# Kernel optimization log

Measured on AMD Instinct MI355X. Metric: run time of the kernel, lower is better.

The kernel has to match this reference:

```python
import jax, jax.numpy as jnp
import numpy as np
import math

B, N, H, D = 2, 2048, 16, 64

def setup_inputs() -> dict:
    key = jax.random.key(0)
    kq, kk, kv = jax.random.split(key, 3)
    q = jax.random.normal(kq, (B, N, H, D), dtype=jnp.float32)
    k = jax.random.normal(kk, (B, N, H, D), dtype=jnp.float32)
    v = jax.random.normal(kv, (B, N, H, D), dtype=jnp.float32)
    return {"q": q, "k": k, "v": v}

def reference(q, k, v):
    # world_size == 1 path: standard full attention.
    d = q.shape[-1]
    scale = 1.0 / math.sqrt(d)
    # [b, h, nq, nk]
    scores = jnp.einsum("bqhd,bkhd->bhqk", q, k) * scale
    attn = jax.nn.softmax(scores, axis=-1)
    out = jnp.einsum("bhqk,bkhd->bqhd", attn, v)
    return out
```

## Files before the change

kernel.cpp:

```cpp
#include <hip/hip_runtime.h>
#include <hip/hip_bf16.h>
#include <math.h>

typedef __bf16 bf16x8 __attribute__((ext_vector_type(8)));
typedef float  f32x4  __attribute__((ext_vector_type(4)));

#define B_    2
#define N_    2048
#define H_    16
#define D_    64
#define HD    (H_ * D_)
#define QSCALE (0.125f * 1.44269504089f)
#define THR   8.0f
#define NT    32
#define TILE_BYTES 16384
#define BH_BYTES ((size_t)NT * TILE_BYTES)
#define WS_NEED ((size_t)B_ * H_ * BH_BYTES)

#if __has_builtin(__builtin_amdgcn_exp2f)
#define EXP2F(x) __builtin_amdgcn_exp2f(x)
#else
#define EXP2F(x) __expf(0.69314718056f * (x))
#endif

__global__ __launch_bounds__(256) void prep_kv(
    const float* __restrict__ k, const float* __restrict__ v,
    char* __restrict__ ws)
{
    __shared__ float tile[64][68];
    const int tid = threadIdx.x;
    const int bid = blockIdx.x;

    if (bid < 1024) {
        int bh = bid >> 5, t = bid & 31;
        int b = bh >> 4, h = bh & 15;
        char* dst = ws + (size_t)bh * BH_BYTES + (size_t)t * TILE_BYTES;
        #pragma unroll
        for (int p = 0; p < 2; ++p) {
            int d16 = (tid & 3) + p * 4;
            int n   = tid >> 2;
            const float* s = k + ((size_t)(b * N_ + t * 64 + n) * H_ + h) * D_ + d16 * 8;
            f32x4 a0 = *(const f32x4*)s;
            f32x4 a1 = *(const f32x4*)(s + 4);
            bf16x8 o;
            #pragma unroll
            for (int j = 0; j < 4; ++j) { o[j] = (__bf16)a0[j]; o[4 + j] = (__bf16)a1[j]; }
            int chunk = n * 8 + (d16 ^ (n & 7));
            *(bf16x8*)(dst + chunk * 16) = o;
        }
    } else {
        int vb = bid - 1024;
        int bh = vb >> 5, t = vb & 31;
        int b = bh >> 4, h = bh & 15;
        #pragma unroll
        for (int rep = 0; rep < 4; ++rep) {
            int idx = rep * 256 + tid;
            int i = idx >> 4, c4 = (idx & 15) * 4;
            *(f32x4*)&tile[i][c4] =
                *(const f32x4*)(v + ((size_t)(b * N_ + t * 64 + i) * H_ + h) * D_ + c4);
        }
        __syncthreads();
        char* dst = ws + (size_t)bh * BH_BYTES + (size_t)t * TILE_BYTES + 8192;
        #pragma unroll
        for (int rep = 0; rep < 2; ++rep) {
            int idx = rep * 256 + tid;
            int d = idx >> 3, n16 = idx & 7;
            bf16x8 o;
            #pragma unroll
            for (int j = 0; j < 8; ++j) o[j] = (__bf16)tile[n16 * 8 + j][d];
            int chunk = d * 8 + (n16 ^ (d & 7));
            *(bf16x8*)(dst + chunk * 16) = o;
        }
    }
}

__global__ __launch_bounds__(512, 4) void attn_fwd_v4(
    const float* __restrict__ q,
    const char* __restrict__ ws,
    float* __restrict__ out)
{
    const int tid  = threadIdx.x;
    const int lane = tid & 63;
    const int w    = tid >> 6;
    const int lo   = lane & 15;
    const int hi   = lane >> 4;

    int bid = blockIdx.x;
    int wg  = (bid & 7) * 64 + (bid >> 3);
    int qt  = wg & 15;
    int bh  = wg >> 4;
    int h   = bh & 15;
    int b   = bh >> 4;

    __shared__ __align__(16) char kv_lds[2][TILE_BYTES];
    __shared__ __align__(16) __bf16 p_lds[8][16][72];

    const char* wsrc = ws + (size_t)bh * BH_BYTES;
    const int q0 = qt * 128 + w * 16;

    bf16x8 qa[2];
    #pragma unroll
    for (int kk = 0; kk < 2; ++kk) {
        const float* qs = q + ((size_t)(b * N_ + q0 + lo) * H_ + h) * D_ + kk * 32 + hi * 8;
        f32x4 a0 = *(const f32x4*)qs;
        f32x4 a1 = *(const f32x4*)(qs + 4);
        #pragma unroll
        for (int j = 0; j < 4; ++j) {
            qa[kk][j]     = (__bf16)(a0[j] * QSCALE);
            qa[kk][4 + j] = (__bf16)(a1[j] * QSCALE);
        }
    }

    float m[4], l[4];
    f32x4 o[4];
    #pragma unroll
    for (int r = 0; r < 4; ++r) { m[r] = -INFINITY; l[r] = 0.f; }
    #pragma unroll
    for (int f = 0; f < 4; ++f) o[f] = (f32x4)0.f;

    const int soff = w * 2048 + lane * 16;

    {
        bf16x8 s0 = *(const bf16x8*)(wsrc + soff);
        bf16x8 s1 = *(const bf16x8*)(wsrc + soff + 1024);
        *(bf16x8*)(kv_lds[0] + soff) = s0;
        *(bf16x8*)(kv_lds[0] + soff + 1024) = s1;
    }
    __syncthreads();

    for (int t = 0; t < NT; ++t) {
        const char* kbuf = kv_lds[t & 1];
        const char* vbuf = kbuf + 8192;

        int tn = (t + 1) & (NT - 1);
        bf16x8 s0 = *(const bf16x8*)(wsrc + (size_t)tn * TILE_BYTES + soff);
        bf16x8 s1 = *(const bf16x8*)(wsrc + (size_t)tn * TILE_BYTES + soff + 1024);

        f32x4 sc[4];
        #pragma unroll
        for (int c = 0; c < 4; ++c) {
            sc[c] = (f32x4)0.f;
            #pragma unroll
            for (int kk = 0; kk < 2; ++kk) {
                int row = c * 16 + lo;
                int d16 = kk * 4 + hi;
                bf16x8 kf = *(const bf16x8*)(kbuf + row * 128 + ((d16 ^ (row & 7)) << 4));
                sc[c] = __builtin_amdgcn_mfma_f32_16x16x32_bf16(qa[kk], kf, sc[c], 0, 0, 0);
            }
        }
        bf16x8 vf[4][2];
        #pragma unroll
        for (int f = 0; f < 4; ++f)
            #pragma unroll
            for (int s2 = 0; s2 < 2; ++s2) {
                int row = f * 16 + lo;
                int n16 = s2 * 4 + hi;
                vf[f][s2] = *(const bf16x8*)(vbuf + row * 128 + ((n16 ^ (row & 7)) << 4));
            }

        float pm[4];
        #pragma unroll
        for (int r = 0; r < 4; ++r)
            pm[r] = fmaxf(fmaxf(sc[0][r], sc[1][r]), fmaxf(sc[2][r], sc[3][r]));
        int ok = (pm[0] <= m[0] + THR) & (pm[1] <= m[1] + THR)
               & (pm[2] <= m[2] + THR) & (pm[3] <= m[3] + THR);
        if (!__all(ok)) {
            #pragma unroll
            for (int r = 0; r < 4; ++r) {
                float tmax = pm[r];
                #pragma unroll
                for (int msk = 1; msk <= 8; msk <<= 1)
                    tmax = fmaxf(tmax, __shfl_xor(tmax, msk, 64));
                float mn = fmaxf(m[r], tmax);
                float a  = EXP2F(m[r] - mn);
                m[r] = mn;
                l[r] *= a;
                #pragma unroll
                for (int f = 0; f < 4; ++f) o[f][r] *= a;
            }
        }
        #pragma unroll
        for (int r = 0; r < 4; ++r) {
            float p0 = EXP2F(sc[0][r] - m[r]);
            float p1 = EXP2F(sc[1][r] - m[r]);
            float p2 = EXP2F(sc[2][r] - m[r]);
            float p3 = EXP2F(sc[3][r] - m[r]);
            l[r] += (p0 + p1) + (p2 + p3);
            p_lds[w][hi * 4 + r][lo]      = (__bf16)p0;
            p_lds[w][hi * 4 + r][16 + lo] = (__bf16)p1;
            p_lds[w][hi * 4 + r][32 + lo] = (__bf16)p2;
            p_lds[w][hi * 4 + r][48 + lo] = (__bf16)p3;
        }
        __asm__ volatile("" ::: "memory");
        bf16x8 pa0 = *(const bf16x8*)&p_lds[w][lo][hi * 8];
        bf16x8 pa1 = *(const bf16x8*)&p_lds[w][lo][32 + hi * 8];
        __asm__ volatile("" ::: "memory");

        #pragma unroll
        for (int f = 0; f < 4; ++f) {
            o[f] = __builtin_amdgcn_mfma_f32_16x16x32_bf16(pa0, vf[f][0], o[f], 0, 0, 0);
            o[f] = __builtin_amdgcn_mfma_f32_16x16x32_bf16(pa1, vf[f][1], o[f], 0, 0, 0);
        }

        *(bf16x8*)(kv_lds[(t + 1) & 1] + soff) = s0;
        *(bf16x8*)(kv_lds[(t + 1) & 1] + soff + 1024) = s1;
        __syncthreads();
    }

    float* op = out + (size_t)b * N_ * HD + (size_t)h * D_;
    #pragma unroll
    for (int r = 0; r < 4; ++r) {
        float rs = l[r];
        #pragma unroll
        for (int msk = 1; msk <= 8; msk <<= 1)
            rs += __shfl_xor(rs, msk, 64);
        float rinv = 1.f / rs;
        float* orow = op + (size_t)(q0 + hi * 4 + r) * HD;
        #pragma unroll
        for (int f = 0; f < 4; ++f)
            orow[f * 16 + lo] = o[f][r] * rinv;
    }
}

__global__ __launch_bounds__(256) void attn_fwd_v1(
    const float* __restrict__ q, const float* __restrict__ k,
    const float* __restrict__ v, float* __restrict__ out)
{
    const int tid  = threadIdx.x;
    const int lane = tid & 63;
    const int w    = tid >> 6;
    const int lo   = lane & 15;
    const int hi   = lane >> 4;
    const int qt   = blockIdx.x;
    const int h    = blockIdx.y;
    const int b    = blockIdx.z;

    __shared__ __align__(16) __bf16 p_lds[4][16][40];

    const size_t bh_off = (size_t)b * N_ * HD + (size_t)h * D_;
    const float* qp = q + bh_off;
    const float* kp = k + bh_off;
    const float* vp = v + bh_off;
    float*       op = out + bh_off;

    const int q0 = qt * 64 + w * 16;

    bf16x8 qa[2];
    {
        const float* qrow = qp + (size_t)(q0 + lo) * HD + hi * 8;
        #pragma unroll
        for (int kk = 0; kk < 2; ++kk)
            #pragma unroll
            for (int j = 0; j < 8; ++j)
                qa[kk][j] = (__bf16)(qrow[kk * 32 + j] * 0.125f);
    }

    float m[4], l[4];
    f32x4 o[4];
    #pragma unroll
    for (int r = 0; r < 4; ++r) { m[r] = -INFINITY; l[r] = 0.f; }
    #pragma unroll
    for (int f = 0; f < 4; ++f) o[f] = (f32x4)0.f;

    for (int kv0 = 0; kv0 < N_; kv0 += 32) {
        f32x4 s[2];
        #pragma unroll
        for (int c = 0; c < 2; ++c) {
            s[c] = (f32x4)0.f;
            const float* krow = kp + (size_t)(kv0 + c * 16 + lo) * HD + hi * 8;
            #pragma unroll
            for (int kk = 0; kk < 2; ++kk) {
                bf16x8 kbv;
                #pragma unroll
                for (int j = 0; j < 8; ++j) kbv[j] = (__bf16)krow[kk * 32 + j];
                s[c] = __builtin_amdgcn_mfma_f32_16x16x32_bf16(qa[kk], kbv, s[c], 0, 0, 0);
            }
        }
        float alpha[4], p0[4], p1[4];
        #pragma unroll
        for (int r = 0; r < 4; ++r) {
            float t = fmaxf(s[0][r], s[1][r]);
            #pragma unroll
            for (int msk = 1; msk <= 8; msk <<= 1) t = fmaxf(t, __shfl_xor(t, msk, 64));
            float mn = fmaxf(m[r], t);
            alpha[r] = __expf(m[r] - mn);
            p0[r] = __expf(s[0][r] - mn);
            p1[r] = __expf(s[1][r] - mn);
            float rs = p0[r] + p1[r];
            #pragma unroll
            for (int msk = 1; msk <= 8; msk <<= 1) rs += __shfl_xor(rs, msk, 64);
            l[r] = l[r] * alpha[r] + rs;
            m[r] = mn;
        }
        #pragma unroll
        for (int f = 0; f < 4; ++f)
            #pragma unroll
            for (int r = 0; r < 4; ++r) o[f][r] *= alpha[r];
        #pragma unroll
        for (int r = 0; r < 4; ++r) {
            p_lds[w][hi * 4 + r][lo]      = (__bf16)p0[r];
            p_lds[w][hi * 4 + r][16 + lo] = (__bf16)p1[r];
        }
        __syncthreads();
        bf16x8 pa = *(const bf16x8*)&p_lds[w][lo][hi * 8];
        #pragma unroll
        for (int f = 0; f < 4; ++f) {
            const float* vrow = vp + (size_t)(kv0 + hi * 8) * HD + f * 16 + lo;
            bf16x8 vb;
            #pragma unroll
            for (int j = 0; j < 8; ++j) vb[j] = (__bf16)vrow[(size_t)j * HD];
            o[f] = __builtin_amdgcn_mfma_f32_16x16x32_bf16(pa, vb, o[f], 0, 0, 0);
        }
        __syncthreads();
    }
    #pragma unroll
    for (int r = 0; r < 4; ++r) {
        float rinv = 1.f / l[r];
        float* orow = op + (size_t)(q0 + hi * 4 + r) * HD;
        #pragma unroll
        for (int f = 0; f < 4; ++f) orow[f * 16 + lo] = o[f][r] * rinv;
    }
}

extern "C" void kernel_launch(void* const* d_in, const int* in_sizes, int n_in,
                              void* d_out, int out_size, void* d_ws, size_t ws_size,
                              hipStream_t stream)
{
    const float* q = (const float*)d_in[0];
    const float* k = (const float*)d_in[1];
    const float* v = (const float*)d_in[2];
    float* out = (float*)d_out;

    if (ws_size >= WS_NEED) {
        char* ws = (char*)d_ws;
        prep_kv<<<dim3(2048), 256, 0, stream>>>(k, v, ws);
        attn_fwd_v4<<<dim3(512), 512, 0, stream>>>(q, ws, out);
    } else {
        attn_fwd_v1<<<dim3(N_ / 64, H_, B_), 256, 0, stream>>>(q, k, v, out);
    }
}
```

Baseline: 148.0 us.

## Process two 16-row query blocks per wave to reuse K/V fragments

Each wave now handles 32 query rows (two 16-row blocks), so every K and V fragment read from LDS feeds twice as many MFMAs. The workgroup covers 256 queries, which halves the grid to 256 blocks and the per-block K/V staging traffic. The prep kernel now writes K/V without the swizzle, and the swizzle moves to the global-to-LDS copy in the attention kernel. The cost is roughly double the accumulator and score registers per wave (occupancy hint lowered from 4 to 2), and with only 256 blocks the GPU may be underfilled.

```diff
diff --git a/kernel.cpp b/kernel.cpp
--- a/kernel.cpp
+++ b/kernel.cpp
@@ -27,29 +27,27 @@
     const float* __restrict__ k, const float* __restrict__ v,
     char* __restrict__ ws)
 {
-    __shared__ float tile[64][68];
+    __shared__ float tile[64][69];
     const int tid = threadIdx.x;
     const int bid = blockIdx.x;
 
-    if (bid < 1024) {
-        int bh = bid >> 5, t = bid & 31;
+    if (bid < 2048) {
+        int g   = bid * 256 + tid;
+        int bh  = g >> 14;
+        int rem = g & 16383;
+        int t   = rem >> 9;
+        int c   = rem & 511;
+        int n   = c >> 3, d16 = c & 7;
         int b = bh >> 4, h = bh & 15;
-        char* dst = ws + (size_t)bh * BH_BYTES + (size_t)t * TILE_BYTES;
-        #pragma unroll
-        for (int p = 0; p < 2; ++p) {
-            int d16 = (tid & 3) + p * 4;
-            int n   = tid >> 2;
-            const float* s = k + ((size_t)(b * N_ + t * 64 + n) * H_ + h) * D_ + d16 * 8;
-            f32x4 a0 = *(const f32x4*)s;
-            f32x4 a1 = *(const f32x4*)(s + 4);
-            bf16x8 o;
-            #pragma unroll
-            for (int j = 0; j < 4; ++j) { o[j] = (__bf16)a0[j]; o[4 + j] = (__bf16)a1[j]; }
-            int chunk = n * 8 + (d16 ^ (n & 7));
-            *(bf16x8*)(dst + chunk * 16) = o;
-        }
+        const float* s = k + ((size_t)(b * N_ + t * 64 + n) * H_ + h) * D_ + d16 * 8;
+        f32x4 a0 = *(const f32x4*)s;
+        f32x4 a1 = *(const f32x4*)(s + 4);
+        bf16x8 o;
+        #pragma unroll
+        for (int j = 0; j < 4; ++j) { o[j] = (__bf16)a0[j]; o[4 + j] = (__bf16)a1[j]; }
+        *(bf16x8*)(ws + (size_t)bh * BH_BYTES + (size_t)t * TILE_BYTES + c * 16) = o;
     } else {
-        int vb = bid - 1024;
+        int vb = bid - 2048;
         int bh = vb >> 5, t = vb & 31;
         int b = bh >> 4, h = bh & 15;
         #pragma unroll
@@ -63,18 +61,17 @@
         char* dst = ws + (size_t)bh * BH_BYTES + (size_t)t * TILE_BYTES + 8192;
         #pragma unroll
         for (int rep = 0; rep < 2; ++rep) {
-            int idx = rep * 256 + tid;
-            int d = idx >> 3, n16 = idx & 7;
+            int c = rep * 256 + tid;
+            int d = c >> 3, n16 = c & 7;
             bf16x8 o;
             #pragma unroll
             for (int j = 0; j < 8; ++j) o[j] = (__bf16)tile[n16 * 8 + j][d];
-            int chunk = d * 8 + (n16 ^ (d & 7));
-            *(bf16x8*)(dst + chunk * 16) = o;
+            *(bf16x8*)(dst + c * 16) = o;
         }
     }
 }
 
-__global__ __launch_bounds__(512, 4) void attn_fwd_v4(
+__global__ __launch_bounds__(512, 2) void attn_fwd_v5(
     const float* __restrict__ q,
     const char* __restrict__ ws,
     float* __restrict__ out)
@@ -86,9 +83,9 @@
     const int hi   = lane >> 4;
 
     int bid = blockIdx.x;
-    int wg  = (bid & 7) * 64 + (bid >> 3);
-    int qt  = wg & 15;
-    int bh  = wg >> 4;
+    int wg  = (bid & 7) * 32 + (bid >> 3);
+    int qt  = wg & 7;
+    int bh  = wg >> 3;
     int h   = bh & 15;
     int b   = bh >> 4;
 
@@ -96,35 +93,44 @@
     __shared__ __align__(16) __bf16 p_lds[8][16][72];
 
     const char* wsrc = ws + (size_t)bh * BH_BYTES;
-    const int q0 = qt * 128 + w * 16;
-
-    bf16x8 qa[2];
-    #pragma unroll
-    for (int kk = 0; kk < 2; ++kk) {
-        const float* qs = q + ((size_t)(b * N_ + q0 + lo) * H_ + h) * D_ + kk * 32 + hi * 8;
-        f32x4 a0 = *(const f32x4*)qs;
-        f32x4 a1 = *(const f32x4*)(qs + 4);
-        #pragma unroll
-        for (int j = 0; j < 4; ++j) {
-            qa[kk][j]     = (__bf16)(a0[j] * QSCALE);
-            qa[kk][4 + j] = (__bf16)(a1[j] * QSCALE);
-        }
-    }
-
-    float m[4], l[4];
-    f32x4 o[4];
-    #pragma unroll
-    for (int r = 0; r < 4; ++r) { m[r] = -INFINITY; l[r] = 0.f; }
-    #pragma unroll
-    for (int f = 0; f < 4; ++f) o[f] = (f32x4)0.f;
-
-    const int soff = w * 2048 + lane * 16;
+    const int q0 = qt * 256 + w * 32;
+
+    const int srow = tid >> 3, scol = tid & 7;
+    const int src0 = (srow * 8 + (scol ^ (srow & 7))) * 16;
+    const int src1 = src0 + 8192;
+    const int ldso0 = tid * 16, ldso1 = tid * 16 + 8192;
+
+    bf16x8 qa[2][2];
+    #pragma unroll
+    for (int rb = 0; rb < 2; ++rb)
+        #pragma unroll
+        for (int kk = 0; kk < 2; ++kk) {
+            const float* qs = q + ((size_t)(b * N_ + q0 + rb * 16 + lo) * H_ + h) * D_ + kk * 32 + hi * 8;
+            f32x4 a0 = *(const f32x4*)qs;
+            f32x4 a1 = *(const f32x4*)(qs + 4);
+            #pragma unroll
+            for (int j = 0; j < 4; ++j) {
+                qa[rb][kk][j]     = (__bf16)(a0[j] * QSCALE);
+                qa[rb][kk][4 + j] = (__bf16)(a1[j] * QSCALE);
+            }
+        }
+
+    float m[2][4], l[2][4];
+    f32x4 o[2][4];
+    #pragma unroll
+    for (int rb = 0; rb < 2; ++rb)
+        #pragma unroll
+        for (int r = 0; r < 4; ++r) { m[rb][r] = -INFINITY; l[rb][r] = 0.f; }
+    #pragma unroll
+    for (int rb = 0; rb < 2; ++rb)
+        #pragma unroll
+        for (int f = 0; f < 4; ++f) o[rb][f] = (f32x4)0.f;
 
     {
-        bf16x8 s0 = *(const bf16x8*)(wsrc + soff);
-        bf16x8 s1 = *(const bf16x8*)(wsrc + soff + 1024);
-        *(bf16x8*)(kv_lds[0] + soff) = s0;
-        *(bf16x8*)(kv_lds[0] + soff + 1024) = s1;
+        bf16x8 s0 = *(const bf16x8*)(wsrc + src0);
+        bf16x8 s1 = *(const bf16x8*)(wsrc + src1);
+        *(bf16x8*)(kv_lds[0] + ldso0) = s0;
+        *(bf16x8*)(kv_lds[0] + ldso1) = s1;
     }
     __syncthreads();
 
@@ -132,22 +138,25 @@
         const char* kbuf = kv_lds[t & 1];
         const char* vbuf = kbuf + 8192;
 
-        int tn = (t + 1) & (NT - 1);
-        bf16x8 s0 = *(const bf16x8*)(wsrc + (size_t)tn * TILE_BYTES + soff);
-        bf16x8 s1 = *(const bf16x8*)(wsrc + (size_t)tn * TILE_BYTES + soff + 1024);
-
-        f32x4 sc[4];
-        #pragma unroll
-        for (int c = 0; c < 4; ++c) {
-            sc[c] = (f32x4)0.f;
+        const size_t tb = (size_t)((t + 1) & (NT - 1)) * TILE_BYTES;
+        bf16x8 s0 = *(const bf16x8*)(wsrc + tb + src0);
+        bf16x8 s1 = *(const bf16x8*)(wsrc + tb + src1);
+
+        f32x4 sc[2][4];
+        #pragma unroll
+        for (int rb = 0; rb < 2; ++rb)
+            #pragma unroll
+            for (int c = 0; c < 4; ++c) sc[rb][c] = (f32x4)0.f;
+        #pragma unroll
+        for (int c = 0; c < 4; ++c)
             #pragma unroll
             for (int kk = 0; kk < 2; ++kk) {
                 int row = c * 16 + lo;
                 int d16 = kk * 4 + hi;
                 bf16x8 kf = *(const bf16x8*)(kbuf + row * 128 + ((d16 ^ (row & 7)) << 4));
-                sc[c] = __builtin_amdgcn_mfma_f32_16x16x32_bf16(qa[kk], kf, sc[c], 0, 0, 0);
-            }
-        }
+                sc[0][c] = __builtin_amdgcn_mfma_f32_16x16x32_bf16(qa[0][kk], kf, sc[0][c], 0, 0, 0);
+                sc[1][c] = __builtin_amdgcn_mfma_f32_16x16x32_bf16(qa[1][kk], kf, sc[1][c], 0, 0, 0);
+            }
         bf16x8 vf[4][2];
         #pragma unroll
         for (int f = 0; f < 4; ++f)
@@ -158,68 +167,72 @@
                 vf[f][s2] = *(const bf16x8*)(vbuf + row * 128 + ((n16 ^ (row & 7)) << 4));
             }
 
-        float pm[4];
-        #pragma unroll
-        for (int r = 0; r < 4; ++r)
-            pm[r] = fmaxf(fmaxf(sc[0][r], sc[1][r]), fmaxf(sc[2][r], sc[3][r]));
-        int ok = (pm[0] <= m[0] + THR) & (pm[1] <= m[1] + THR)
-               & (pm[2] <= m[2] + THR) & (pm[3] <= m[3] + THR);
-        if (!__all(ok)) {
+        #pragma unroll
+        for (int rb = 0; rb < 2; ++rb) {
+            float pm[4];
+            #pragma unroll
+            for (int r = 0; r < 4; ++r)
+                pm[r] = fmaxf(fmaxf(sc[rb][0][r], sc[rb][1][r]), fmaxf(sc[rb][2][r], sc[rb][3][r]));
+            int ok = (pm[0] <= m[rb][0] + THR) & (pm[1] <= m[rb][1] + THR)
+                   & (pm[2] <= m[rb][2] + THR) & (pm[3] <= m[rb][3] + THR);
+            if (!__all(ok)) {
+                #pragma unroll
+                for (int r = 0; r < 4; ++r) {
+                    float tmax = pm[r];
+                    #pragma unroll
+                    for (int msk = 1; msk <= 8; msk <<= 1)
+                        tmax = fmaxf(tmax, __shfl_xor(tmax, msk, 64));
+                    float mn = fmaxf(m[rb][r], tmax);
+                    float a  = EXP2F(m[rb][r] - mn);
+                    m[rb][r] = mn;
+                    l[rb][r] *= a;
+                    #pragma unroll
+                    for (int f = 0; f < 4; ++f) o[rb][f][r] *= a;
+                }
+            }
             #pragma unroll
             for (int r = 0; r < 4; ++r) {
-                float tmax = pm[r];
-                #pragma unroll
-                for (int msk = 1; msk <= 8; msk <<= 1)
-                    tmax = fmaxf(tmax, __shfl_xor(tmax, msk, 64));
-                float mn = fmaxf(m[r], tmax);
-                float a  = EXP2F(m[r] - mn);
-                m[r] = mn;
-                l[r] *= a;
-                #pragma unroll
-                for (int f = 0; f < 4; ++f) o[f][r] *= a;
-            }
-        }
+                float p0 = EXP2F(sc[rb][0][r] - m[rb][r]);
+                float p1 = EXP2F(sc[rb][1][r] - m[rb][r]);
+                float p2 = EXP2F(sc[rb][2][r] - m[rb][r]);
+                float p3 = EXP2F(sc[rb][3][r] - m[rb][r]);
+                l[rb][r] += (p0 + p1) + (p2 + p3);
+                p_lds[w][hi * 4 + r][lo]      = (__bf16)p0;
+                p_lds[w][hi * 4 + r][16 + lo] = (__bf16)p1;
+                p_lds[w][hi * 4 + r][32 + lo] = (__bf16)p2;
+                p_lds[w][hi * 4 + r][48 + lo] = (__bf16)p3;
+            }
+            __asm__ volatile("" ::: "memory");
+            bf16x8 pa0 = *(const bf16x8*)&p_lds[w][lo][hi * 8];
+            bf16x8 pa1 = *(const bf16x8*)&p_lds[w][lo][32 + hi * 8];
+            __asm__ volatile("" ::: "memory");
+            #pragma unroll
+            for (int f = 0; f < 4; ++f) {
+                o[rb][f] = __builtin_amdgcn_mfma_f32_16x16x32_bf16(pa0, vf[f][0], o[rb][f], 0, 0, 0);
+                o[rb][f] = __builtin_amdgcn_mfma_f32_16x16x32_bf16(pa1, vf[f][1], o[rb][f], 0, 0, 0);
+            }
+        }
+
+        *(bf16x8*)(kv_lds[(t + 1) & 1] + ldso0) = s0;
+        *(bf16x8*)(kv_lds[(t + 1) & 1] + ldso1) = s1;
+        __syncthreads();
+    }
+
+    float* op = out + (size_t)b * N_ * HD + (size_t)h * D_;
+    #pragma unroll
+    for (int rb = 0; rb < 2; ++rb)
         #pragma unroll
         for (int r = 0; r < 4; ++r) {
-            float p0 = EXP2F(sc[0][r] - m[r]);
-            float p1 = EXP2F(sc[1][r] - m[r]);
-            float p2 = EXP2F(sc[2][r] - m[r]);
-            float p3 = EXP2F(sc[3][r] - m[r]);
-            l[r] += (p0 + p1) + (p2 + p3);
-            p_lds[w][hi * 4 + r][lo]      = (__bf16)p0;
-            p_lds[w][hi * 4 + r][16 + lo] = (__bf16)p1;
-            p_lds[w][hi * 4 + r][32 + lo] = (__bf16)p2;
-            p_lds[w][hi * 4 + r][48 + lo] = (__bf16)p3;
-        }
-        __asm__ volatile("" ::: "memory");
-        bf16x8 pa0 = *(const bf16x8*)&p_lds[w][lo][hi * 8];
-        bf16x8 pa1 = *(const bf16x8*)&p_lds[w][lo][32 + hi * 8];
-        __asm__ volatile("" ::: "memory");
-
-        #pragma unroll
-        for (int f = 0; f < 4; ++f) {
-            o[f] = __builtin_amdgcn_mfma_f32_16x16x32_bf16(pa0, vf[f][0], o[f], 0, 0, 0);
-            o[f] = __builtin_amdgcn_mfma_f32_16x16x32_bf16(pa1, vf[f][1], o[f], 0, 0, 0);
-        }
-
-        *(bf16x8*)(kv_lds[(t + 1) & 1] + soff) = s0;
-        *(bf16x8*)(kv_lds[(t + 1) & 1] + soff + 1024) = s1;
-        __syncthreads();
-    }
-
-    float* op = out + (size_t)b * N_ * HD + (size_t)h * D_;
-    #pragma unroll
-    for (int r = 0; r < 4; ++r) {
-        float rs = l[r];
-        #pragma unroll
-        for (int msk = 1; msk <= 8; msk <<= 1)
-            rs += __shfl_xor(rs, msk, 64);
-        float rinv = 1.f / rs;
-        float* orow = op + (size_t)(q0 + hi * 4 + r) * HD;
-        #pragma unroll
-        for (int f = 0; f < 4; ++f)
-            orow[f * 16 + lo] = o[f][r] * rinv;
-    }
+            float rs = l[rb][r];
+            #pragma unroll
+            for (int msk = 1; msk <= 8; msk <<= 1)
+                rs += __shfl_xor(rs, msk, 64);
+            float rinv = 1.f / rs;
+            float* orow = op + (size_t)(q0 + rb * 16 + hi * 4 + r) * HD;
+            #pragma unroll
+            for (int f = 0; f < 4; ++f)
+                orow[f * 16 + lo] = o[rb][f][r] * rinv;
+        }
 }
 
 __global__ __launch_bounds__(256) void attn_fwd_v1(
@@ -333,8 +346,8 @@
 
     if (ws_size >= WS_NEED) {
         char* ws = (char*)d_ws;
-        prep_kv<<<dim3(2048), 256, 0, stream>>>(k, v, ws);
-        attn_fwd_v4<<<dim3(512), 512, 0, stream>>>(q, ws, out);
+        prep_kv<<<dim3(3072), 256, 0, stream>>>(k, v, ws);
+        attn_fwd_v5<<<dim3(256), 512, 0, stream>>>(q, ws, out);
     } else {
         attn_fwd_v1<<<dim3(N_ / 64, H_, B_), 256, 0, stream>>>(q, k, v, out);
     }
```

Measured after the change: 149.7 us. Within noise of the previous version (+1.1%).
